# Kernel tuning notes

Measured on AMD Instinct MI355X. Metric: run time of the kernel, lower is better.

The kernel has to match this reference:

```python
import jax, jax.numpy as jnp
import numpy as np

IN_C, DIM, OUT_C, N_PIECES = 3, 256, 256, 20
BATCH, SET_N = 16, 128


def _xavier(k, shape, fan_in, fan_out):
    limit = float(np.sqrt(6.0 / (fan_in + fan_out)))
    return jax.random.uniform(k, shape, jnp.float32, -limit, limit)


def setup_inputs() -> dict:
    key = jax.random.key(0)
    ks = jax.random.split(key, 9)
    return {
        "x": jax.random.normal(ks[0], (BATCH, IN_C, SET_N), jnp.float32),
        "conv1_w": _xavier(ks[1], (DIM, IN_C), IN_C, DIM),
        "conv1_b": jnp.zeros((DIM,), jnp.float32),
        "conv2_w": _xavier(ks[2], (DIM, DIM), DIM, DIM),
        "conv2_b": jnp.zeros((DIM,), jnp.float32),
        "pool_w": jax.random.normal(ks[3], (DIM, N_PIECES + 1), jnp.float32) * 0.1,
        "lin1_w": _xavier(ks[4], (DIM, DIM), DIM, DIM),
        "lin1_b": jnp.zeros((DIM,), jnp.float32),
        "lin2_w": _xavier(ks[5], (OUT_C, DIM), DIM, OUT_C),
        "lin2_b": jnp.zeros((OUT_C,), jnp.float32),
        "cls1_w": _xavier(ks[6], (OUT_C, OUT_C), OUT_C, OUT_C),
        "cls1_b": jnp.zeros((OUT_C,), jnp.float32),
        "cls2_w": _xavier(ks[7], (10, OUT_C), OUT_C, 10),
        "cls2_b": jnp.zeros((10,), jnp.float32),
    }


def _fspool(x, pool_w, tau=1.0):
    # x: (B, C, N); pool_w: (C, N_PIECES+1). n is None -> full sets, mask is all ones.
    B, C, N = x.shape
    # piecewise-linear continuous weights evaluated at ratios i/(N-1)
    ratios = jnp.clip(jnp.arange(N, dtype=x.dtype) / max(N - 1, 1), 0.0, 1.0)  # (N,)
    idx_f = N_PIECES * ratios
    idx = jnp.floor(idx_f).astype(jnp.int32)
    frac = idx_f - idx.astype(x.dtype)
    left = pool_w[:, idx]                                   # (C, N)
    right = pool_w[:, jnp.clip(idx + 1, 0, N_PIECES)]       # (C, N)
    w = (1.0 - frac) * left + frac * right                  # (C, N)
    # relaxed continuous sort (NeuralSort / deterministic_sort), descending
    s = x.reshape(B * C, N, 1)
    A = jnp.abs(s - jnp.swapaxes(s, 1, 2))                  # (BC, N, N)
    Bsum = A.sum(axis=2, keepdims=True)                     # == A @ 1 1^T rowsums, (BC, N, 1)
    scaling = (N + 1 - 2 * (jnp.arange(N) + 1)).astype(x.dtype)  # (N,)
    Cmat = s * scaling[None, None, :]                       # (BC, N, N)
    P = jax.nn.softmax(jnp.swapaxes(Cmat - Bsum, 1, 2) / tau, axis=-1)  # (BC, N, N)
    xs = jnp.matmul(P, s).reshape(B, C, N)                  # soft-sorted, descending
    pooled = (xs * w[None]).sum(axis=2)                     # (B, C)
    return pooled, P


def reference(x, conv1_w, conv1_b, conv2_w, conv2_b, pool_w,
              lin1_w, lin1_b, lin2_w, lin2_b, cls1_w, cls1_b, cls2_w, cls2_b):
    # conv1x1 stack: (B, IN_C, N) -> (B, DIM, N)
    h = jnp.einsum('dc,bcn->bdn', conv1_w, x) + conv1_b[None, :, None]
    h = jax.nn.relu(h)
    h = jnp.einsum('dc,bcn->bdn', conv2_w, h) + conv2_b[None, :, None]
    pooled, _ = _fspool(h, pool_w)                          # (B, DIM)
    z = jax.nn.relu(pooled @ lin1_w.T + lin1_b)
    z = z @ lin2_w.T + lin2_b                               # (B, OUT_C)
    z = jax.nn.relu(z @ cls1_w.T + cls1_b)
    return z @ cls2_w.T + cls2_b                            # (B, 10)
```

## Files before the change

### kernel.cpp

```cpp
#include <hip/hip_runtime.h>
#include <math.h>


#if __has_builtin(__builtin_amdgcn_exp2f)
#define EXP2F(x) __builtin_amdgcn_exp2f(x)
#else
#define EXP2F(x) exp2f(x)
#endif

__global__ __launch_bounds__(256) void conv12_kernel(
    const float* __restrict__ x, const float* __restrict__ w1,
    const float* __restrict__ b1, const float* __restrict__ W2,
    const float* __restrict__ b2, float* __restrict__ H2)
{
    __shared__ float xs[3][64];
    __shared__ float As[16][32];
    __shared__ float Bs[16][64];

    int tid = threadIdx.x;
    int bx  = blockIdx.x;
    int d0  = blockIdx.y * 32;
    int b   = bx >> 1;
    int n0  = (bx & 1) * 64;

    if (tid < 192) {
        int c = tid >> 6, n = tid & 63;
        xs[c][n] = x[b * 384 + c * 128 + n0 + n];
    }
    __syncthreads();

    int tx = tid & 15, ty = tid >> 4;
    int dl = tid & 31, kk2 = tid >> 5;
    float acc[2][4] = {};

    for (int k0 = 0; k0 < 256; k0 += 16) {
        float2 wv = *(const float2*)(W2 + (d0 + dl) * 256 + k0 + kk2 * 2);
        As[kk2 * 2 + 0][dl] = wv.x;
        As[kk2 * 2 + 1][dl] = wv.y;
        #pragma unroll
        for (int q = 0; q < 4; q++) {
            int idx = tid + 256 * q;
            int krel = idx >> 6, nl = idx & 63;
            int k = k0 + krel;
            float h = fmaf(w1[k * 3 + 0], xs[0][nl],
                      fmaf(w1[k * 3 + 1], xs[1][nl],
                      fmaf(w1[k * 3 + 2], xs[2][nl], b1[k])));
            Bs[krel][nl] = fmaxf(h, 0.0f);
        }
        __syncthreads();
        #pragma unroll
        for (int kk = 0; kk < 16; kk++) {
            float2 a  = *(const float2*)(&As[kk][ty * 2]);
            float4 bv = *(const float4*)(&Bs[kk][tx * 4]);
            acc[0][0] = fmaf(a.x, bv.x, acc[0][0]);
            acc[0][1] = fmaf(a.x, bv.y, acc[0][1]);
            acc[0][2] = fmaf(a.x, bv.z, acc[0][2]);
            acc[0][3] = fmaf(a.x, bv.w, acc[0][3]);
            acc[1][0] = fmaf(a.y, bv.x, acc[1][0]);
            acc[1][1] = fmaf(a.y, bv.y, acc[1][1]);
            acc[1][2] = fmaf(a.y, bv.z, acc[1][2]);
            acc[1][3] = fmaf(a.y, bv.w, acc[1][3]);
        }
        __syncthreads();
    }

    #pragma unroll
    for (int i = 0; i < 2; i++) {
        int d = d0 + ty * 2 + i;
        float bias = b2[d];
        float4 o = make_float4(acc[i][0] + bias, acc[i][1] + bias,
                               acc[i][2] + bias, acc[i][3] + bias);
        *(float4*)(H2 + b * 32768 + d * 128 + n0 + tx * 4) = o;
    }
}

__device__ __forceinline__ float pool_weight(const float* __restrict__ pw, int j)
{
    float ratio = (float)j / 127.0f;
    float idx_f = 20.0f * ratio;
    int idx = (int)idx_f;
    float frac = idx_f - (float)idx;
    int idx2 = idx + 1 > 20 ? 20 : idx + 1;
    return (1.0f - frac) * pw[idx] + frac * pw[idx2];
}

__global__ __launch_bounds__(256) void fspool_kernel(
    const float* __restrict__ s_glob,
    const float* __restrict__ pool_w,
    float* __restrict__ pooled)
{
    const float LOG2E = 1.4426950408889634f;
    int wave = threadIdx.x >> 6;
    int lane = threadIdx.x & 63;
    int row  = blockIdx.x * 4 + wave;

    __shared__ float2 sb[4][128];

    const float* srow = s_glob + row * 128;
    float2 sv = *(const float2*)(srow + lane * 2);
    sb[wave][lane * 2]     = make_float2(sv.x, 0.0f);
    sb[wave][lane * 2 + 1] = make_float2(sv.y, 0.0f);
    __syncthreads();

    float si0 = sb[wave][lane].x;
    float si1 = sb[wave][lane + 64].x;
    float B0 = 0.0f, B1 = 0.0f;
    #pragma unroll 8
    for (int j = 0; j < 128; j++) {
        float sj = sb[wave][j].x;
        B0 += fabsf(si0 - sj);
        B1 += fabsf(si1 - sj);
    }
    sb[wave][lane].y      = B0 * LOG2E;
    sb[wave][lane + 64].y = B1 * LOG2E;
    __syncthreads();

    float scal0 = (float)(127 - 2 * lane) * LOG2E;
    float scal1 = (float)(127 - 2 * (lane + 64)) * LOG2E;
    float m0 = -1e30f, m1 = -1e30f;
    #pragma unroll 8
    for (int i = 0; i < 128; i++) {
        float2 v = sb[wave][i];
        m0 = fmaxf(m0, fmaf(v.x, scal0, -v.y));
        m1 = fmaxf(m1, fmaf(v.x, scal1, -v.y));
    }
    float se0 = 0.0f, sd0 = 0.0f, se1 = 0.0f, sd1 = 0.0f;
    #pragma unroll 4
    for (int i = 0; i < 128; i++) {
        float2 v = sb[wave][i];
        float e0 = EXP2F(fmaf(v.x, scal0, -v.y) - m0);
        float e1 = EXP2F(fmaf(v.x, scal1, -v.y) - m1);
        se0 += e0; sd0 = fmaf(e0, v.x, sd0);
        se1 += e1; sd1 = fmaf(e1, v.x, sd1);
    }
    float xs0 = sd0 / se0;
    float xs1 = sd1 / se1;

    int c = row & 255;
    const float* pw = pool_w + c * 21;
    float part = xs0 * pool_weight(pw, lane) + xs1 * pool_weight(pw, lane + 64);

    #pragma unroll
    for (int off = 32; off > 0; off >>= 1)
        part += __shfl_xor(part, off);
    if (lane == 0) pooled[row] = part;
}

__device__ __forceinline__ void dense1024(
    const float* __restrict__ W, const float* __restrict__ Bv,
    const float* in_lds, float* out_lds, int tid, bool do_relu)
{
    int o = tid >> 2, p = tid & 3;
    const float* wr = W + o * 256 + p * 64;
    const float* ir = in_lds + p * 64;
    float acc = 0.0f;
    #pragma unroll
    for (int k = 0; k < 64; k += 4) {
        float4 wv = *(const float4*)(wr + k);
        float4 iv = *(const float4*)(ir + k);
        acc = fmaf(wv.x, iv.x, acc);
        acc = fmaf(wv.y, iv.y, acc);
        acc = fmaf(wv.z, iv.z, acc);
        acc = fmaf(wv.w, iv.w, acc);
    }
    acc += __shfl_xor(acc, 1);
    acc += __shfl_xor(acc, 2);
    if (p == 0) {
        acc += Bv[o];
        out_lds[o] = do_relu ? fmaxf(acc, 0.0f) : acc;
    }
}

__global__ __launch_bounds__(1024) void tail_kernel(
    const float* __restrict__ pooled,
    const float* __restrict__ W1, const float* __restrict__ B1,
    const float* __restrict__ W2, const float* __restrict__ B2,
    const float* __restrict__ W3, const float* __restrict__ B3,
    const float* __restrict__ W4, const float* __restrict__ B4,
    float* __restrict__ out)
{
    __shared__ float za[256], zb[256];
    int b = blockIdx.x, tid = threadIdx.x;
    if (tid < 256) za[tid] = pooled[b * 256 + tid];
    __syncthreads();
    dense1024(W1, B1, za, zb, tid, true);
    __syncthreads();
    dense1024(W2, B2, zb, za, tid, false);
    __syncthreads();
    dense1024(W3, B3, za, zb, tid, true);
    __syncthreads();
    if (tid < 640) {
        int o = tid >> 6, kb = tid & 63;
        float4 wv = *(const float4*)(W4 + o * 256 + kb * 4);
        float4 zv = *(const float4*)(zb + kb * 4);
        float p = fmaf(wv.x, zv.x, fmaf(wv.y, zv.y,
                  fmaf(wv.z, zv.z, wv.w * zv.w)));
        #pragma unroll
        for (int off = 32; off > 0; off >>= 1)
            p += __shfl_xor(p, off);
        if (kb == 0) out[b * 10 + o] = p + B4[o];
    }
}

extern "C" void kernel_launch(void* const* d_in, const int* in_sizes, int n_in,
                              void* d_out, int out_size, void* d_ws, size_t ws_size,
                              hipStream_t stream)
{
    (void)in_sizes; (void)n_in; (void)out_size; (void)ws_size;
    const float* x       = (const float*)d_in[0];
    const float* conv1_w = (const float*)d_in[1];
    const float* conv1_b = (const float*)d_in[2];
    const float* conv2_w = (const float*)d_in[3];
    const float* conv2_b = (const float*)d_in[4];
    const float* pool_w  = (const float*)d_in[5];
    const float* lin1_w  = (const float*)d_in[6];
    const float* lin1_b  = (const float*)d_in[7];
    const float* lin2_w  = (const float*)d_in[8];
    const float* lin2_b  = (const float*)d_in[9];
    const float* cls1_w  = (const float*)d_in[10];
    const float* cls1_b  = (const float*)d_in[11];
    const float* cls2_w  = (const float*)d_in[12];
    const float* cls2_b  = (const float*)d_in[13];
    float* out = (float*)d_out;

    float* ws     = (float*)d_ws;
    float* H2     = ws;
    float* pooled = ws + 524288;

    conv12_kernel<<<dim3(32, 8), 256, 0, stream>>>(x, conv1_w, conv1_b,
                                                   conv2_w, conv2_b, H2);
    fspool_kernel<<<1024, 256, 0, stream>>>(H2, pool_w, pooled);
    tail_kernel<<<16, 1024, 0, stream>>>(pooled,
        lin1_w, lin1_b, lin2_w, lin2_b, cls1_w, cls1_b, cls2_w, cls2_b, out);
}
```

Measured before the change: 62.22 us.

## Fuse conv stack and FSPool soft-sort into one kernel via shared memory

Merges the conv1/conv2 GEMM kernel and the FSPool soft-sort kernel into a single 1024-thread kernel. Each block computes 16 channels × 128 set elements of one batch and keeps them in LDS for the sort, so the 2 MB H2 intermediate never goes to global memory and one launch is removed. In exchange there are only 256 blocks with a smaller GEMM tile per thread (2 outputs), which lowers per-thread reuse, and the conv1 activations are recomputed for each channel block.

Measured after the change: 64.44 us. 1.04x slower.

```diff
diff --git a/kernel.cpp b/kernel.cpp
--- a/kernel.cpp
+++ b/kernel.cpp
@@ -7,72 +7,6 @@
 #else
 #define EXP2F(x) exp2f(x)
 #endif
-
-__global__ __launch_bounds__(256) void conv12_kernel(
-    const float* __restrict__ x, const float* __restrict__ w1,
-    const float* __restrict__ b1, const float* __restrict__ W2,
-    const float* __restrict__ b2, float* __restrict__ H2)
-{
-    __shared__ float xs[3][64];
-    __shared__ float As[16][32];
-    __shared__ float Bs[16][64];
-
-    int tid = threadIdx.x;
-    int bx  = blockIdx.x;
-    int d0  = blockIdx.y * 32;
-    int b   = bx >> 1;
-    int n0  = (bx & 1) * 64;
-
-    if (tid < 192) {
-        int c = tid >> 6, n = tid & 63;
-        xs[c][n] = x[b * 384 + c * 128 + n0 + n];
-    }
-    __syncthreads();
-
-    int tx = tid & 15, ty = tid >> 4;
-    int dl = tid & 31, kk2 = tid >> 5;
-    float acc[2][4] = {};
-
-    for (int k0 = 0; k0 < 256; k0 += 16) {
-        float2 wv = *(const float2*)(W2 + (d0 + dl) * 256 + k0 + kk2 * 2);
-        As[kk2 * 2 + 0][dl] = wv.x;
-        As[kk2 * 2 + 1][dl] = wv.y;
-        #pragma unroll
-        for (int q = 0; q < 4; q++) {
-            int idx = tid + 256 * q;
-            int krel = idx >> 6, nl = idx & 63;
-            int k = k0 + krel;
-            float h = fmaf(w1[k * 3 + 0], xs[0][nl],
-                      fmaf(w1[k * 3 + 1], xs[1][nl],
-                      fmaf(w1[k * 3 + 2], xs[2][nl], b1[k])));
-            Bs[krel][nl] = fmaxf(h, 0.0f);
-        }
-        __syncthreads();
-        #pragma unroll
-        for (int kk = 0; kk < 16; kk++) {
-            float2 a  = *(const float2*)(&As[kk][ty * 2]);
-            float4 bv = *(const float4*)(&Bs[kk][tx * 4]);
-            acc[0][0] = fmaf(a.x, bv.x, acc[0][0]);
-            acc[0][1] = fmaf(a.x, bv.y, acc[0][1]);
-            acc[0][2] = fmaf(a.x, bv.z, acc[0][2]);
-            acc[0][3] = fmaf(a.x, bv.w, acc[0][3]);
-            acc[1][0] = fmaf(a.y, bv.x, acc[1][0]);
-            acc[1][1] = fmaf(a.y, bv.y, acc[1][1]);
-            acc[1][2] = fmaf(a.y, bv.z, acc[1][2]);
-            acc[1][3] = fmaf(a.y, bv.w, acc[1][3]);
-        }
-        __syncthreads();
-    }
-
-    #pragma unroll
-    for (int i = 0; i < 2; i++) {
-        int d = d0 + ty * 2 + i;
-        float bias = b2[d];
-        float4 o = make_float4(acc[i][0] + bias, acc[i][1] + bias,
-                               acc[i][2] + bias, acc[i][3] + bias);
-        *(float4*)(H2 + b * 32768 + d * 128 + n0 + tx * 4) = o;
-    }
-}
 
 __device__ __forceinline__ float pool_weight(const float* __restrict__ pw, int j)
 {
@@ -84,50 +18,94 @@
     return (1.0f - frac) * pw[idx] + frac * pw[idx2];
 }
 
-__global__ __launch_bounds__(256) void fspool_kernel(
-    const float* __restrict__ s_glob,
-    const float* __restrict__ pool_w,
+__global__ __launch_bounds__(1024) void fused_kernel(
+    const float* __restrict__ x,  const float* __restrict__ w1,
+    const float* __restrict__ b1, const float* __restrict__ W2,
+    const float* __restrict__ b2, const float* __restrict__ pool_w,
     float* __restrict__ pooled)
 {
+    __shared__ float4 xs4[128];
+    __shared__ float4 w1p[256];
+    __shared__ float  As[16][16];
+    __shared__ float  Bs[16][128];
+    __shared__ float2 sbB[16][128];
+
     const float LOG2E = 1.4426950408889634f;
-    int wave = threadIdx.x >> 6;
-    int lane = threadIdx.x & 63;
-    int row  = blockIdx.x * 4 + wave;
-
-    __shared__ float2 sb[4][128];
-
-    const float* srow = s_glob + row * 128;
-    float2 sv = *(const float2*)(srow + lane * 2);
-    sb[wave][lane * 2]     = make_float2(sv.x, 0.0f);
-    sb[wave][lane * 2 + 1] = make_float2(sv.y, 0.0f);
-    __syncthreads();
-
-    float si0 = sb[wave][lane].x;
-    float si1 = sb[wave][lane + 64].x;
+    int tid = threadIdx.x;
+    int b   = blockIdx.x >> 4;
+    int d0  = (blockIdx.x & 15) << 4;
+
+    if (tid < 128) {
+        int n = tid;
+        xs4[n] = make_float4(x[b*384 + n], x[b*384 + 128 + n],
+                             x[b*384 + 256 + n], 0.0f);
+    } else if (tid < 384) {
+        int k = tid - 128;
+        w1p[k] = make_float4(w1[k*3], w1[k*3+1], w1[k*3+2], b1[k]);
+    }
+    __syncthreads();
+
+    int ty = tid >> 6;
+    int tx = tid & 63;
+    float acc0 = 0.0f, acc1 = 0.0f;
+
+    for (int k0 = 0; k0 < 256; k0 += 16) {
+        if (tid < 256) {
+            int dl = tid >> 4, kk = tid & 15;
+            As[kk][dl] = W2[(d0 + dl)*256 + k0 + kk];
+        }
+        #pragma unroll
+        for (int q = 0; q < 2; q++) {
+            int krel = ((tid >> 7) << 1) + q;
+            int nl   = tid & 127;
+            float4 w  = w1p[k0 + krel];
+            float4 xv = xs4[nl];
+            float h = fmaf(w.x, xv.x, fmaf(w.y, xv.y, fmaf(w.z, xv.z, w.w)));
+            Bs[krel][nl] = fmaxf(h, 0.0f);
+        }
+        __syncthreads();
+        #pragma unroll
+        for (int kk = 0; kk < 16; kk++) {
+            float a = As[kk][ty];
+            float2 bv = *(const float2*)(&Bs[kk][tx*2]);
+            acc0 = fmaf(a, bv.x, acc0);
+            acc1 = fmaf(a, bv.y, acc1);
+        }
+        __syncthreads();
+    }
+
+    float bias = b2[d0 + ty];
+    sbB[ty][tx*2 + 0].x = acc0 + bias;
+    sbB[ty][tx*2 + 1].x = acc1 + bias;
+    __syncthreads();
+
+    int w = ty, lane = tx;
+
+    float si0 = sbB[w][lane].x;
+    float si1 = sbB[w][lane + 64].x;
     float B0 = 0.0f, B1 = 0.0f;
     #pragma unroll 8
     for (int j = 0; j < 128; j++) {
-        float sj = sb[wave][j].x;
+        float sj = sbB[w][j].x;
         B0 += fabsf(si0 - sj);
         B1 += fabsf(si1 - sj);
     }
-    sb[wave][lane].y      = B0 * LOG2E;
-    sb[wave][lane + 64].y = B1 * LOG2E;
-    __syncthreads();
-
-    float scal0 = (float)(127 - 2 * lane) * LOG2E;
-    float scal1 = (float)(127 - 2 * (lane + 64)) * LOG2E;
+    sbB[w][lane].y      = B0 * LOG2E;
+    sbB[w][lane + 64].y = B1 * LOG2E;
+
+    float scal0 = (float)(127 - 2*lane) * LOG2E;
+    float scal1 = (float)(127 - 2*(lane + 64)) * LOG2E;
     float m0 = -1e30f, m1 = -1e30f;
     #pragma unroll 8
     for (int i = 0; i < 128; i++) {
-        float2 v = sb[wave][i];
+        float2 v = sbB[w][i];
         m0 = fmaxf(m0, fmaf(v.x, scal0, -v.y));
         m1 = fmaxf(m1, fmaf(v.x, scal1, -v.y));
     }
     float se0 = 0.0f, sd0 = 0.0f, se1 = 0.0f, sd1 = 0.0f;
     #pragma unroll 4
     for (int i = 0; i < 128; i++) {
-        float2 v = sb[wave][i];
+        float2 v = sbB[w][i];
         float e0 = EXP2F(fmaf(v.x, scal0, -v.y) - m0);
         float e1 = EXP2F(fmaf(v.x, scal1, -v.y) - m1);
         se0 += e0; sd0 = fmaf(e0, v.x, sd0);
@@ -136,14 +114,14 @@
     float xs0 = sd0 / se0;
     float xs1 = sd1 / se1;
 
-    int c = row & 255;
+    int c = d0 + w;
     const float* pw = pool_w + c * 21;
     float part = xs0 * pool_weight(pw, lane) + xs1 * pool_weight(pw, lane + 64);
 
     #pragma unroll
     for (int off = 32; off > 0; off >>= 1)
         part += __shfl_xor(part, off);
-    if (lane == 0) pooled[row] = part;
+    if (lane == 0) pooled[b * 256 + c] = part;
 }
 
 __device__ __forceinline__ void dense1024(
@@ -223,13 +201,10 @@
     const float* cls2_b  = (const float*)d_in[13];
     float* out = (float*)d_out;
 
-    float* ws     = (float*)d_ws;
-    float* H2     = ws;
-    float* pooled = ws + 524288;
-
-    conv12_kernel<<<dim3(32, 8), 256, 0, stream>>>(x, conv1_w, conv1_b,
-                                                   conv2_w, conv2_b, H2);
-    fspool_kernel<<<1024, 256, 0, stream>>>(H2, pool_w, pooled);
+    float* pooled = (float*)d_ws;
+
+    fused_kernel<<<256, 1024, 0, stream>>>(x, conv1_w, conv1_b,
+                                           conv2_w, conv2_b, pool_w, pooled);
     tail_kernel<<<16, 1024, 0, stream>>>(pooled,
         lin1_w, lin1_b, lin2_w, lin2_b, cls1_w, cls1_b, cls2_w, cls2_b, out);
 }
```

## Double grid parallelism in conv and fspool kernels, one element per thread

Applied to the files above, without the earlier changes.

The conv2 GEMM tile shrinks from 32 to 16 output channels, so the grid doubles to 512 blocks and each thread now computes 4 outputs instead of 8. In the soft-sort pooling kernel each row is split across two waves, so each thread handles one element instead of two, and the 2048 blocks combine their halves through shared memory. The inner loops now use float4 LDS reads with four independent accumulators and a shared max for the softmax. The aim is more waves in flight and shorter per-thread dependency chains on a GPU with many CUs, at the cost of more redundant conv1 recomputation, extra syncs and less register reuse.

Measured after the change: 59.69 us. -4.1%, faster.

```diff
diff --git a/kernel.cpp b/kernel.cpp
--- a/kernel.cpp
+++ b/kernel.cpp
@@ -14,12 +14,12 @@
     const float* __restrict__ b2, float* __restrict__ H2)
 {
     __shared__ float xs[3][64];
-    __shared__ float As[16][32];
+    __shared__ float As[16][16];
     __shared__ float Bs[16][64];
 
     int tid = threadIdx.x;
     int bx  = blockIdx.x;
-    int d0  = blockIdx.y * 32;
+    int d0  = blockIdx.y * 16;
     int b   = bx >> 1;
     int n0  = (bx & 1) * 64;
 
@@ -30,16 +30,16 @@
     __syncthreads();
 
     int tx = tid & 15, ty = tid >> 4;
-    int dl = tid & 31, kk2 = tid >> 5;
-    float acc[2][4] = {};
+    float acc[4] = {};
 
     for (int k0 = 0; k0 < 256; k0 += 16) {
-        float2 wv = *(const float2*)(W2 + (d0 + dl) * 256 + k0 + kk2 * 2);
-        As[kk2 * 2 + 0][dl] = wv.x;
-        As[kk2 * 2 + 1][dl] = wv.y;
+        {
+            int dl = tid & 15, kk = tid >> 4;
+            As[kk][dl] = W2[(d0 + dl) * 256 + k0 + kk];
+        }
         #pragma unroll
         for (int q = 0; q < 4; q++) {
-            int idx = tid + 256 * q;
+            int idx = q * 256 + tid;
             int krel = idx >> 6, nl = idx & 63;
             int k = k0 + krel;
             float h = fmaf(w1[k * 3 + 0], xs[0][nl],
@@ -50,28 +50,21 @@
         __syncthreads();
         #pragma unroll
         for (int kk = 0; kk < 16; kk++) {
-            float2 a  = *(const float2*)(&As[kk][ty * 2]);
+            float a  = As[kk][ty];
             float4 bv = *(const float4*)(&Bs[kk][tx * 4]);
-            acc[0][0] = fmaf(a.x, bv.x, acc[0][0]);
-            acc[0][1] = fmaf(a.x, bv.y, acc[0][1]);
-            acc[0][2] = fmaf(a.x, bv.z, acc[0][2]);
-            acc[0][3] = fmaf(a.x, bv.w, acc[0][3]);
-            acc[1][0] = fmaf(a.y, bv.x, acc[1][0]);
-            acc[1][1] = fmaf(a.y, bv.y, acc[1][1]);
-            acc[1][2] = fmaf(a.y, bv.z, acc[1][2]);
-            acc[1][3] = fmaf(a.y, bv.w, acc[1][3]);
+            acc[0] = fmaf(a, bv.x, acc[0]);
+            acc[1] = fmaf(a, bv.y, acc[1]);
+            acc[2] = fmaf(a, bv.z, acc[2]);
+            acc[3] = fmaf(a, bv.w, acc[3]);
         }
         __syncthreads();
     }
 
-    #pragma unroll
-    for (int i = 0; i < 2; i++) {
-        int d = d0 + ty * 2 + i;
-        float bias = b2[d];
-        float4 o = make_float4(acc[i][0] + bias, acc[i][1] + bias,
-                               acc[i][2] + bias, acc[i][3] + bias);
-        *(float4*)(H2 + b * 32768 + d * 128 + n0 + tx * 4) = o;
-    }
+    int d = d0 + ty;
+    float bias = b2[d];
+    float4 o = make_float4(acc[0] + bias, acc[1] + bias,
+                           acc[2] + bias, acc[3] + bias);
+    *(float4*)(H2 + b * 32768 + d * 128 + n0 + tx * 4) = o;
 }
 
 __device__ __forceinline__ float pool_weight(const float* __restrict__ pw, int j)
@@ -84,66 +77,80 @@
     return (1.0f - frac) * pw[idx] + frac * pw[idx2];
 }
 
-__global__ __launch_bounds__(256) void fspool_kernel(
+__global__ __launch_bounds__(256, 8) void fspool_kernel(
     const float* __restrict__ s_glob,
     const float* __restrict__ pool_w,
     float* __restrict__ pooled)
 {
     const float LOG2E = 1.4426950408889634f;
-    int wave = threadIdx.x >> 6;
-    int lane = threadIdx.x & 63;
-    int row  = blockIdx.x * 4 + wave;
-
-    __shared__ float2 sb[4][128];
-
-    const float* srow = s_glob + row * 128;
-    float2 sv = *(const float2*)(srow + lane * 2);
-    sb[wave][lane * 2]     = make_float2(sv.x, 0.0f);
-    sb[wave][lane * 2 + 1] = make_float2(sv.y, 0.0f);
-    __syncthreads();
-
-    float si0 = sb[wave][lane].x;
-    float si1 = sb[wave][lane + 64].x;
-    float B0 = 0.0f, B1 = 0.0f;
-    #pragma unroll 8
-    for (int j = 0; j < 128; j++) {
-        float sj = sb[wave][j].x;
-        B0 += fabsf(si0 - sj);
-        B1 += fabsf(si1 - sj);
-    }
-    sb[wave][lane].y      = B0 * LOG2E;
-    sb[wave][lane + 64].y = B1 * LOG2E;
-    __syncthreads();
-
-    float scal0 = (float)(127 - 2 * lane) * LOG2E;
-    float scal1 = (float)(127 - 2 * (lane + 64)) * LOG2E;
-    float m0 = -1e30f, m1 = -1e30f;
-    #pragma unroll 8
-    for (int i = 0; i < 128; i++) {
-        float2 v = sb[wave][i];
-        m0 = fmaxf(m0, fmaf(v.x, scal0, -v.y));
-        m1 = fmaxf(m1, fmaf(v.x, scal1, -v.y));
-    }
-    float se0 = 0.0f, sd0 = 0.0f, se1 = 0.0f, sd1 = 0.0f;
+    __shared__ float ss[2][128];
+    __shared__ float bb[2][128];
+    __shared__ float part[2][2];
+
+    int tid  = threadIdx.x;
+    int wave = tid >> 6;
+    int rl   = wave >> 1;
+    int half = wave & 1;
+    int lane = tid & 63;
+    int i    = half * 64 + lane;
+    int row  = blockIdx.x * 2 + rl;
+
+    float si = s_glob[row * 128 + i];
+    ss[rl][i] = si;
+    __syncthreads();
+
+    float a0 = 0.f, a1 = 0.f, a2 = 0.f, a3 = 0.f;
     #pragma unroll 4
-    for (int i = 0; i < 128; i++) {
-        float2 v = sb[wave][i];
-        float e0 = EXP2F(fmaf(v.x, scal0, -v.y) - m0);
-        float e1 = EXP2F(fmaf(v.x, scal1, -v.y) - m1);
-        se0 += e0; sd0 = fmaf(e0, v.x, sd0);
-        se1 += e1; sd1 = fmaf(e1, v.x, sd1);
-    }
-    float xs0 = sd0 / se0;
-    float xs1 = sd1 / se1;
+    for (int j = 0; j < 128; j += 4) {
+        float4 sv = *(const float4*)(&ss[rl][j]);
+        a0 += fabsf(si - sv.x);
+        a1 += fabsf(si - sv.y);
+        a2 += fabsf(si - sv.z);
+        a3 += fabsf(si - sv.w);
+    }
+    bb[rl][i] = ((a0 + a1) + (a2 + a3)) * LOG2E;
+    __syncthreads();
+
+    float scal = (float)(127 - 2 * i) * LOG2E;
+    float m0 = -1e30f, m1 = -1e30f, m2 = -1e30f, m3 = -1e30f;
+    #pragma unroll 4
+    for (int k = 0; k < 128; k += 4) {
+        float4 sv = *(const float4*)(&ss[rl][k]);
+        float4 bv = *(const float4*)(&bb[rl][k]);
+        m0 = fmaxf(m0, fmaf(sv.x, scal, -bv.x));
+        m1 = fmaxf(m1, fmaf(sv.y, scal, -bv.y));
+        m2 = fmaxf(m2, fmaf(sv.z, scal, -bv.z));
+        m3 = fmaxf(m3, fmaf(sv.w, scal, -bv.w));
+    }
+    float m = fmaxf(fmaxf(m0, m1), fmaxf(m2, m3));
+
+    float se0 = 0.f, se1 = 0.f, se2 = 0.f, se3 = 0.f;
+    float sd0 = 0.f, sd1 = 0.f, sd2 = 0.f, sd3 = 0.f;
+    #pragma unroll 4
+    for (int k = 0; k < 128; k += 4) {
+        float4 sv = *(const float4*)(&ss[rl][k]);
+        float4 bv = *(const float4*)(&bb[rl][k]);
+        float e0 = EXP2F(fmaf(sv.x, scal, -bv.x) - m);
+        float e1 = EXP2F(fmaf(sv.y, scal, -bv.y) - m);
+        float e2 = EXP2F(fmaf(sv.z, scal, -bv.z) - m);
+        float e3 = EXP2F(fmaf(sv.w, scal, -bv.w) - m);
+        se0 += e0; se1 += e1; se2 += e2; se3 += e3;
+        sd0 = fmaf(e0, sv.x, sd0);
+        sd1 = fmaf(e1, sv.y, sd1);
+        sd2 = fmaf(e2, sv.z, sd2);
+        sd3 = fmaf(e3, sv.w, sd3);
+    }
+    float xs = ((sd0 + sd1) + (sd2 + sd3)) / ((se0 + se1) + (se2 + se3));
 
     int c = row & 255;
-    const float* pw = pool_w + c * 21;
-    float part = xs0 * pool_weight(pw, lane) + xs1 * pool_weight(pw, lane + 64);
-
+    float p = xs * pool_weight(pool_w + c * 21, i);
     #pragma unroll
     for (int off = 32; off > 0; off >>= 1)
-        part += __shfl_xor(part, off);
-    if (lane == 0) pooled[row] = part;
+        p += __shfl_xor(p, off);
+    if (lane == 0) part[rl][half] = p;
+    __syncthreads();
+    if (tid < 2)
+        pooled[blockIdx.x * 2 + tid] = part[tid][0] + part[tid][1];
 }
 
 __device__ __forceinline__ void dense1024(
@@ -227,9 +234,9 @@
     float* H2     = ws;
     float* pooled = ws + 524288;
 
-    conv12_kernel<<<dim3(32, 8), 256, 0, stream>>>(x, conv1_w, conv1_b,
-                                                   conv2_w, conv2_b, H2);
-    fspool_kernel<<<1024, 256, 0, stream>>>(H2, pool_w, pooled);
+    conv12_kernel<<<dim3(32, 16), 256, 0, stream>>>(x, conv1_w, conv1_b,
+                                                    conv2_w, conv2_b, H2);
+    fspool_kernel<<<2048, 256, 0, stream>>>(H2, pool_w, pooled);
     tail_kernel<<<16, 1024, 0, stream>>>(pooled,
         lin1_w, lin1_b, lin2_w, lin2_b, cls1_w, cls1_b, cls2_w, cls2_b, out);
 }
```
